# Optimization experiments

Hardware: AMD Instinct MI355X
Metric: run time of the kernel (lower is better)

## Reference

```python
import jax, jax.numpy as jnp
import numpy as np

SHIFTS = (1, 2)          # _GLOBAL_SHIFTS, all < channels so none filtered
LN_EPS = 1e-5


def _layernorm(x, g, b):
    mu = jnp.mean(x, axis=-1, keepdims=True)
    var = jnp.var(x, axis=-1, keepdims=True)
    return (x - mu) * jax.lax.rsqrt(var + LN_EPS) * g + b


def setup_inputs() -> dict:
    key = jax.random.key(0)
    ks = jax.random.split(key, 4)
    B, H, W, D = 8, 96, 96, 256
    n_comp = 2 * len(SHIFTS)  # full mode: dot + wedge per shift
    x = jax.random.normal(ks[0], (B, H, W, D), dtype=jnp.float32)
    # glorot-uniform style scaling for the two dense kernels
    pk = jax.random.normal(ks[1], (n_comp * D, D), dtype=jnp.float32) * (1.0 / np.sqrt(n_comp * D))
    gk = jax.random.normal(ks[2], (2 * D, D), dtype=jnp.float32) * (1.0 / np.sqrt(2 * D))
    return {
        "x": x,
        "ln_gamma": jnp.ones((D,), jnp.float32),
        "ln_beta": jnp.zeros((D,), jnp.float32),
        "proj_kernel": pk,
        "proj_bias": jnp.zeros((D,), jnp.float32),
        "gate_kernel": gk,
        "gate_bias": jnp.zeros((D,), jnp.float32),
        "gamma": jnp.full((D,), 1e-5, jnp.float32),  # LayerScale init
    }


def reference(x, ln_gamma, ln_beta, proj_kernel, proj_bias,
              gate_kernel, gate_bias, gamma):
    # ---- pre-norm ----
    h_norm = _layernorm(x, ln_gamma, ln_beta)                 # [B,H,W,D]
    # ---- context stream (ctx_mode='diff'): deviation from spatial mean ----
    z_det = h_norm
    z_ctx = h_norm - jnp.mean(h_norm, axis=(1, 2), keepdims=True)
    # ---- sparse rolling Clifford product (cli_mode='full') ----
    feats = []
    for s in SHIFTS:
        ctx_s = jnp.roll(z_ctx, -s, axis=-1)   # Z_ctx[(c+s) % D]
        det_s = jnp.roll(z_det, -s, axis=-1)   # Z_det[(c+s) % D]
        dot = jax.nn.silu(z_det * ctx_s)                      # inner part
        wedge = z_det * ctx_s - z_ctx * det_s                 # bivector part
        feats.append(dot)
        feats.append(wedge)
    feats = jnp.concatenate(feats, axis=-1)                   # [B,H,W,4D]
    g_feat = feats @ proj_kernel + proj_bias                  # [B,H,W,D]
    # ---- gated geometric residual ----
    gate_in = jnp.concatenate([h_norm, g_feat], axis=-1)      # [B,H,W,2D]
    alpha = jax.nn.sigmoid(gate_in @ gate_kernel + gate_bias)
    h_mix = (jax.nn.silu(h_norm) + alpha * g_feat) * gamma    # LayerScale
    # drop_path_rate == 0.0 -> identity; caller-side residual add
    return x + h_mix
```

## Files before the change

### kernel.cpp

```cpp
#include <hip/hip_runtime.h>
#include <hip/hip_bf16.h>

typedef unsigned short u16;
typedef unsigned int   u32;
typedef __attribute__((ext_vector_type(2))) u32   u32x2;
typedef __attribute__((ext_vector_type(4))) float f32x4;
typedef __attribute__((ext_vector_type(4))) u32   u32x4;
typedef __attribute__((ext_vector_type(8))) short bf16x8;

#define HWPIX  9216
#define NPIX   73728
#define LN_EPS 1e-5f
#define MROW   64
#define HSTR   264
#define ASTR   40

template<int N> struct IC { static constexpr int value = N; };

__device__ __forceinline__ u16 f2bf(float f){
  u32 u = __builtin_bit_cast(u32, f);
  u += 0x7fffu + ((u >> 16) & 1u);
  return (u16)(u >> 16);
}
__device__ __forceinline__ u32 pkbf(float lo, float hi){
  u32 d;
  asm("v_cvt_pk_bf16_f32 %0, %1, %2" : "=v"(d) : "v"(lo), "v"(hi));
  return d;
}
__device__ __forceinline__ float lo2f(u32 w){ return __builtin_bit_cast(float, w << 16); }
__device__ __forceinline__ float hi2f(u32 w){ return __builtin_bit_cast(float, w & 0xffff0000u); }
__device__ __forceinline__ float bfu2f(u16 h){ return __builtin_bit_cast(float, (u32)h << 16); }
__device__ __forceinline__ float fsigmoid(float v){ return __fdividef(1.f, 1.f + __expf(-v)); }
__device__ __forceinline__ float fsilu(float v){ return __fdividef(v, 1.f + __expf(-v)); }

__device__ __forceinline__ void gld16(const u16* g, u16* l){
  __builtin_amdgcn_global_load_lds((const __attribute__((address_space(1))) void*)g,
                                   (__attribute__((address_space(3))) void*)l,
                                   16, 0, 0);
}

__global__ __launch_bounds__(256) void wconv(const float* __restrict__ pk,
                                             const float* __restrict__ gk,
                                             u16* __restrict__ wsdot,
                                             u16* __restrict__ wsgate)
{
  int gid = blockIdx.x * 256 + threadIdx.x;
  int t = gid >> 10, S = gid & 1023;
  int q = (S >> 2) & 15, pp = S & 3, w8 = (S >> 6) & 7, rb = S >> 9;
  int n  = rb * 128 + w8 * 16 + q;
  int kq = pp ^ ((q >> 1) & 3);
  const float* W; int k0; u16* dst;
  if (t < 8)       { W = pk; k0 =       t      * 32 + kq * 8; dst = wsdot  + (size_t)t * 8192; }
  else if (t < 16) { W = pk; k0 = 512 + (t-8)  * 32 + kq * 8; dst = wsdot  + (size_t)t * 8192; }
  else             { W = gk; k0 =       (t-16) * 32 + kq * 8; dst = wsgate + (size_t)(t-16) * 8192; }
  u32 ow[4];
  #pragma unroll
  for (int e = 0; e < 4; ++e) {
    float f0 = W[(size_t)(k0 + 2*e)     * 256 + n];
    float f1 = W[(size_t)(k0 + 2*e + 1) * 256 + n];
    ow[e] = (u32)f2bf(f0) | ((u32)f2bf(f1) << 16);
  }
  *(u32x4*)(dst + (size_t)S * 8) = (u32x4){ow[0], ow[1], ow[2], ow[3]};
}

__global__ __launch_bounds__(256) void ln_partial(const float* __restrict__ x,
                                                  const float* __restrict__ g,
                                                  const float* __restrict__ bt,
                                                  float* __restrict__ partial)
{
  const int bh = blockIdx.x;
  const int tid = threadIdx.x;
  const int wv = tid >> 6, lane = tid & 63;
  const float* xrow = x + (size_t)bh * 96 * 256;
  __shared__ float red[4][256];

  f32x4 gv = *(const f32x4*)(g  + lane * 4);
  f32x4 bv = *(const f32x4*)(bt + lane * 4);
  f32x4 acc = {0.f, 0.f, 0.f, 0.f};

  for (int w = wv; w < 96; w += 4) {
    f32x4 v = *(const f32x4*)(xrow + w * 256 + lane * 4);
    float s  = v[0] + v[1] + v[2] + v[3];
    float s2 = v[0]*v[0] + v[1]*v[1] + v[2]*v[2] + v[3]*v[3];
    #pragma unroll
    for (int m = 1; m < 64; m <<= 1) { s += __shfl_xor(s, m); s2 += __shfl_xor(s2, m); }
    float mu  = s * (1.f / 256.f);
    float var = s2 * (1.f / 256.f) - mu * mu;
    float rs  = rsqrtf(var + LN_EPS);
    #pragma unroll
    for (int j = 0; j < 4; ++j) acc[j] += (v[j] - mu) * rs * gv[j] + bv[j];
  }
  *(f32x4*)(&red[wv][lane * 4]) = acc;
  __syncthreads();
  float s = red[0][tid] + red[1][tid] + red[2][tid] + red[3][tid];
  partial[(size_t)bh * 256 + tid] = s;
}

__global__ __launch_bounds__(256) void ln_mean(const float* __restrict__ partial,
                                               float* __restrict__ mean)
{
  int b = blockIdx.x, c = threadIdx.x;
  float s = 0.f;
  for (int h = 0; h < 96; ++h) s += partial[((size_t)b * 96 + h) * 256 + c];
  float m = s * (1.f / 9216.f);
  mean[b * 258 + c] = m;
  if (c < 2) mean[b * 258 + 256 + c] = m;
}

__global__ __launch_bounds__(256) void wfold(const float* __restrict__ pk,
                                             const float* __restrict__ meang,
                                             u16* __restrict__ wsW)
{
  __shared__ float msh[256];
  int gid = blockIdx.x * 256 + threadIdx.x;
  int chunk = gid >> 10;
  int b = chunk >> 3, j = chunk & 7;
  msh[threadIdx.x] = meang[b * 258 + threadIdx.x];
  __syncthreads();
  int S = gid & 1023;
  int q = (S >> 2) & 15, pp = S & 3, w8 = (S >> 6) & 7, rb = S >> 9;
  int n  = rb * 128 + w8 * 16 + q;
  int kq = pp ^ ((q >> 1) & 3);
  u32 ow[4];
  #pragma unroll
  for (int e = 0; e < 4; ++e) {
    float r[2];
    #pragma unroll
    for (int hh = 0; hh < 2; ++hh) {
      int c = j * 32 + kq * 8 + 2 * e + hh;
      int cm1 = (c + 255) & 255, cm2 = (c + 254) & 255;
      int cp1 = (c + 1) & 255,   cp2 = (c + 2) & 255;
      r[hh] = msh[cm1] * pk[(size_t)(256 + cm1) * 256 + n]
            - msh[cp1] * pk[(size_t)(256 + c)   * 256 + n]
            + msh[cm2] * pk[(size_t)(768 + cm2) * 256 + n]
            - msh[cp2] * pk[(size_t)(768 + c)   * 256 + n];
    }
    ow[e] = (u32)f2bf(r[0]) | ((u32)f2bf(r[1]) << 16);
  }
  *(u32x4*)(wsW + (size_t)chunk * 8192 + (size_t)S * 8) = (u32x4){ow[0], ow[1], ow[2], ow[3]};
}

__global__ __launch_bounds__(512, 4) void fused(
    const float* __restrict__ x,
    const float* __restrict__ lng, const float* __restrict__ lnb,
    const u16* __restrict__ wsdot, const u16* __restrict__ wsW,
    const u16* __restrict__ wsgate,
    const float* __restrict__ pbias, const float* __restrict__ gbias,
    const float* __restrict__ gamma, const float* __restrict__ meang,
    float* __restrict__ out)
{
  __shared__ u16 hn[MROW * HSTR];
  __shared__ u16 afg[2][MROW * ASTR];
  __shared__ u16 Bl [2][8192];
  __shared__ float msh[258];

  const int tid  = threadIdx.x;
  const long pix0 = (long)blockIdx.x * MROW;
  const int bat  = (int)(pix0 / HWPIX);

  const int wave = tid >> 6, lane = tid & 63;
  const int wr = wave & 1, wc = wave >> 1;
  const int fr = lane & 15, kq = lane >> 4;
  const int bswz = (kq ^ ((fr >> 1) & 3)) * 8;
  const int br = tid >> 3, bo = (tid & 7) * 4;

  f32x4 acc[2][4];
  #pragma unroll
  for (int i = 0; i < 2; ++i)
    #pragma unroll
    for (int j = 0; j < 4; ++j) acc[i][j] = (f32x4){0.f, 0.f, 0.f, 0.f};
  u32 gfp[2][4][2];

  auto sgptr = [&](auto SG) -> const u16* {
    constexpr int sg = decltype(SG)::value;
    if constexpr      (sg == 0) return wsdot;
    else if constexpr (sg == 1) return wsdot + 8 * 8192;
    else if constexpr (sg == 2) return wsW + (size_t)bat * 65536;
    else if constexpr (sg == 3) return wsgate;
    else                        return wsgate + 8 * 8192;
  };
  auto stageB = [&](auto UC, int buf) {
    constexpr int u = decltype(UC)::value;
    const u16* src = sgptr(IC<(u >> 3)>{}) + (size_t)(u & 7) * 8192 + tid * 8;
    u16* dst = &Bl[buf][wave * 512];
    gld16(src, dst);
    gld16(src + 4096, dst + 4096);
  };

  stageB(IC<0>{}, 0);

  if (tid < 258) msh[tid] = meang[bat * 258 + tid];

  float pbv[4];
  #pragma unroll
  for (int nt = 0; nt < 4; ++nt) pbv[nt] = pbias[wc * 64 + nt * 16 + fr];

  {
    const int p = tid >> 3, o = tid & 7;
    const float* xp = x + (pix0 + p) * 256 + o * 32;
    float s = 0.f, s2 = 0.f;
    #pragma unroll
    for (int i = 0; i < 8; ++i) {
      f32x4 v = *(const f32x4*)(xp + i * 4);
      s  += v[0] + v[1] + v[2] + v[3];
      s2 += v[0]*v[0] + v[1]*v[1] + v[2]*v[2] + v[3]*v[3];
    }
    s += __shfl_xor(s, 1); s2 += __shfl_xor(s2, 1);
    s += __shfl_xor(s, 2); s2 += __shfl_xor(s2, 2);
    s += __shfl_xor(s, 4); s2 += __shfl_xor(s2, 4);
    float mu  = s * (1.f / 256.f);
    float var = s2 * (1.f / 256.f) - mu * mu;
    float rs  = rsqrtf(var + LN_EPS);

    const float* gp = lng + o * 32;
    const float* bp = lnb + o * 32;
    u16* zd = hn + p * HSTR + o * 32;
    #pragma unroll
    for (int i = 0; i < 8; ++i) {
      f32x4 v  = *(const f32x4*)(xp + i * 4);
      f32x4 gg = *(const f32x4*)(gp + i * 4);
      f32x4 bb = *(const f32x4*)(bp + i * 4);
      float h0 = (v[0] - mu) * rs * gg[0] + bb[0];
      float h1 = (v[1] - mu) * rs * gg[1] + bb[1];
      float h2 = (v[2] - mu) * rs * gg[2] + bb[2];
      float h3 = (v[3] - mu) * rs * gg[3] + bb[3];
      u32 d0 = pkbf(h0, h1);
      u32 d1 = pkbf(h2, h3);
      *(u32*)(zd + i * 4)     = d0;
      *(u32*)(zd + i * 4 + 2) = d1;
      if (i == 0 && o == 0) *(u32*)(hn + p * HSTR + 256) = d0;
    }
  }

  auto featsD = [&](auto SC, int w, int buf) {
    constexpr int s = decltype(SC)::value;
    const int cc = w * 32 + bo;
    const u16* zp = hn + br * HSTR + cc;
    u32x2 aa = *(const u32x2*)(zp);
    u32 a2   = *(const u32*)(zp + 4);
    float h0 = lo2f(aa[0]), h1 = hi2f(aa[0]), h2 = lo2f(aa[1]);
    float h3 = hi2f(aa[1]), h4 = lo2f(a2), h5 = hi2f(a2);
    float m0 = msh[cc + s], m1 = msh[cc + s + 1];
    float m2 = msh[cc + s + 2], m3 = msh[cc + s + 3];
    float t0, t1, t2, t3;
    if constexpr (s == 1) { t0 = h1; t1 = h2; t2 = h3; t3 = h4; }
    else                  { t0 = h2; t1 = h3; t2 = h4; t3 = h5; }
    float r0 = fsilu(h0 * (t0 - m0));
    float r1 = fsilu(h1 * (t1 - m1));
    float r2 = fsilu(h2 * (t2 - m2));
    float r3 = fsilu(h3 * (t3 - m3));
    *(u32*)(&afg[buf][br * ASTR + bo])     = pkbf(r0, r1);
    *(u32*)(&afg[buf][br * ASTR + bo + 2]) = pkbf(r2, r3);
  };

  auto gfcopy = [&](auto CGC, int buf) {
    constexpr int cg = decltype(CGC)::value;
    constexpr int par = cg & 1;
    if (wc == (cg >> 1)) {
      #pragma unroll
      for (int v = 0; v < 2; ++v) {
        #pragma unroll
        for (int ai = 0; ai < 2; ++ai)
          #pragma unroll
          for (int rp = 0; rp < 2; ++rp) {
            u32 pw = gfp[ai][par * 2 + v][rp];
            int row0 = wr * 32 + ai * 16 + kq * 4 + rp * 2;
            afg[buf][row0 * ASTR + v * 16 + fr]       = (u16)pw;
            afg[buf][(row0 + 1) * ASTR + v * 16 + fr] = (u16)(pw >> 16);
          }
      }
    }
  };

  auto domfma = [&](const u16* abase, int astr, int buf) {
    bf16x8 av0 = *(const bf16x8*)(abase);
    bf16x8 av1 = *(const bf16x8*)(abase + 16 * astr);
    const u16* bp = &Bl[buf][wc * 2048 + fr * 32 + bswz];
    __builtin_amdgcn_s_setprio(1);
    #pragma unroll
    for (int nt = 0; nt < 4; ++nt) {
      bf16x8 bv = *(const bf16x8*)(bp + nt * 512);
      acc[0][nt] = __builtin_amdgcn_mfma_f32_16x16x32_bf16(av0, bv, acc[0][nt], 0, 0, 0);
      acc[1][nt] = __builtin_amdgcn_mfma_f32_16x16x32_bf16(av1, bv, acc[1][nt], 0, 0, 0);
    }
    __builtin_amdgcn_s_setprio(0);
  };

  asm volatile("s_waitcnt vmcnt(0) lgkmcnt(0)" ::: "memory");
  __builtin_amdgcn_s_barrier();
  featsD(IC<1>{}, 0, 0);
  asm volatile("s_waitcnt lgkmcnt(0)" ::: "memory");
  __builtin_amdgcn_s_barrier();

  auto stepfn = [&](auto SEGC, auto JC) {
    constexpr int SEG = decltype(SEGC)::value;
    constexpr int j   = decltype(JC)::value;
    constexpr int t   = SEG * 8 + j;
    constexpr int cb  = t & 1, nb = cb ^ 1;
    constexpr int u   = t + 1;
    if constexpr (u < 40) stageB(IC<u>{}, nb);
    if constexpr (SEG == 0 || SEG == 1 || SEG == 4)
      domfma(&afg[cb][(wr * 32 + fr) * ASTR + kq * 8], ASTR, cb);
    else
      domfma(&hn[(wr * 32 + fr) * HSTR + j * 32 + kq * 8], HSTR, cb);
    constexpr int useg = u >> 3;
    if constexpr (u < 40) {
      if constexpr      (useg == 0) featsD(IC<1>{}, u & 7, nb);
      else if constexpr (useg == 1) featsD(IC<2>{}, u & 7, nb);
      else if constexpr (useg == 4) gfcopy(IC<u - 32>{}, nb);
    }
    if constexpr (t == 23) {
      #pragma unroll
      for (int nt = 0; nt < 4; ++nt)
        #pragma unroll
        for (int ai = 0; ai < 2; ++ai) {
          f32x4 a = acc[ai][nt];
          gfp[ai][nt][0] = pkbf(a[0] + pbv[nt], a[1] + pbv[nt]);
          gfp[ai][nt][1] = pkbf(a[2] + pbv[nt], a[3] + pbv[nt]);
          acc[ai][nt] = (f32x4){0.f, 0.f, 0.f, 0.f};
        }
    }
    asm volatile("s_waitcnt vmcnt(0) lgkmcnt(0)" ::: "memory");
    __builtin_amdgcn_s_barrier();
  };
  auto runseg = [&](auto SEGC) {
    stepfn(SEGC, IC<0>{}); stepfn(SEGC, IC<1>{});
    stepfn(SEGC, IC<2>{}); stepfn(SEGC, IC<3>{});
    stepfn(SEGC, IC<4>{}); stepfn(SEGC, IC<5>{});
    stepfn(SEGC, IC<6>{}); stepfn(SEGC, IC<7>{});
  };
  runseg(IC<0>{}); runseg(IC<1>{}); runseg(IC<2>{});
  runseg(IC<3>{}); runseg(IC<4>{});

  float gbv[4], gmv[4];
  #pragma unroll
  for (int nt = 0; nt < 4; ++nt) {
    int col = wc * 64 + nt * 16 + fr;
    gbv[nt] = gbias[col]; gmv[nt] = gamma[col];
  }
  #pragma unroll
  for (int ai = 0; ai < 2; ++ai)
    #pragma unroll
    for (int rr = 0; rr < 4; ++rr) {
      const int row = wr * 32 + ai * 16 + kq * 4 + rr;
      const long pix = pix0 + row;
      #pragma unroll
      for (int nt = 0; nt < 4; ++nt) {
        int col = wc * 64 + nt * 16 + fr;
        float xv = x[pix * 256 + col];
        float hh = bfu2f(hn[row * HSTR + col]);
        u32 pw = gfp[ai][nt][rr >> 1];
        float gfv = bfu2f((u16)((rr & 1) ? (pw >> 16) : pw));
        float al = fsigmoid(acc[ai][nt][rr] + gbv[nt]);
        out[pix * 256 + col] = xv + (fsilu(hh) + al * gfv) * gmv[nt];
      }
    }
}

extern "C" void kernel_launch(void* const* d_in, const int* in_sizes, int n_in,
                              void* d_out, int out_size, void* d_ws, size_t ws_size,
                              hipStream_t stream) {
  const float* x     = (const float*)d_in[0];
  const float* lng   = (const float*)d_in[1];
  const float* lnb   = (const float*)d_in[2];
  const float* pk    = (const float*)d_in[3];
  const float* pbias = (const float*)d_in[4];
  const float* gk    = (const float*)d_in[5];
  const float* gbias = (const float*)d_in[6];
  const float* gamma = (const float*)d_in[7];
  float* out = (float*)d_out;

  char* ws = (char*)d_ws;
  u16*   wsdot   = (u16*)ws;
  u16*   wsgate  = (u16*)(ws + 262144);
  float* meang   = (float*)(ws + 524288);
  u16*   wsW     = (u16*)(ws + 532544);
  float* partial = (float*)(ws + 532544);

  wconv<<<128, 256, 0, stream>>>(pk, gk, wsdot, wsgate);
  ln_partial<<<768, 256, 0, stream>>>(x, lng, lnb, partial);
  ln_mean<<<8, 256, 0, stream>>>(partial, meang);
  wfold<<<256, 256, 0, stream>>>(pk, meang, wsW);
  fused<<<NPIX / MROW, 512, 0, stream>>>(x, lng, lnb, wsdot, wsW, wsgate,
                                         pbias, gbias, gamma, meang, out);
}
```

Before: 154.9 us.

## Load B fragments directly to registers and compute dot features per wave

Weight fragments are pre-permuted into MFMA lane order so each wave loads its B operands straight from global memory into registers, double-buffered, in place of staging through shared memory with global_load_lds. The silu dot features are computed in registers per wave from the normalized tile, using a pre-shifted mean table, so the shared feature buffer is used only for the gate segment. This removes most per-step block barriers and the LDS traffic for B and for the dot features. In exchange it raises register pressure and repeats global weight loads for each wave, relying on cache.

```diff
diff --git a/kernel.cpp b/kernel.cpp
--- a/kernel.cpp
+++ b/kernel.cpp
@@ -3,7 +3,6 @@
 
 typedef unsigned short u16;
 typedef unsigned int   u32;
-typedef __attribute__((ext_vector_type(2))) u32   u32x2;
 typedef __attribute__((ext_vector_type(4))) float f32x4;
 typedef __attribute__((ext_vector_type(4))) u32   u32x4;
 typedef __attribute__((ext_vector_type(8))) short bf16x8;
@@ -33,12 +32,6 @@
 __device__ __forceinline__ float fsigmoid(float v){ return __fdividef(1.f, 1.f + __expf(-v)); }
 __device__ __forceinline__ float fsilu(float v){ return __fdividef(v, 1.f + __expf(-v)); }
 
-__device__ __forceinline__ void gld16(const u16* g, u16* l){
-  __builtin_amdgcn_global_load_lds((const __attribute__((address_space(1))) void*)g,
-                                   (__attribute__((address_space(3))) void*)l,
-                                   16, 0, 0);
-}
-
 __global__ __launch_bounds__(256) void wconv(const float* __restrict__ pk,
                                              const float* __restrict__ gk,
                                              u16* __restrict__ wsdot,
@@ -46,18 +39,20 @@
 {
   int gid = blockIdx.x * 256 + threadIdx.x;
   int t = gid >> 10, S = gid & 1023;
-  int q = (S >> 2) & 15, pp = S & 3, w8 = (S >> 6) & 7, rb = S >> 9;
-  int n  = rb * 128 + w8 * 16 + q;
-  int kq = pp ^ ((q >> 1) & 3);
+  int wc = S >> 8, nt = (S >> 6) & 3, lane = S & 63;
+  int fr = lane & 15, kq = lane >> 4;
+  int n  = wc * 64 + nt * 16 + fr;
   const float* W; int k0; u16* dst;
-  if (t < 8)       { W = pk; k0 =       t      * 32 + kq * 8; dst = wsdot  + (size_t)t * 8192; }
-  else if (t < 16) { W = pk; k0 = 512 + (t-8)  * 32 + kq * 8; dst = wsdot  + (size_t)t * 8192; }
-  else             { W = gk; k0 =       (t-16) * 32 + kq * 8; dst = wsgate + (size_t)(t-16) * 8192; }
+  if (t < 8)       { W = pk; k0 =       t      * 32; dst = wsdot  + (size_t)t * 8192; }
+  else if (t < 16) { W = pk; k0 = 512 + (t-8)  * 32; dst = wsdot  + (size_t)t * 8192; }
+  else if (t < 24) { W = gk; k0 =       (t-16) * 32; dst = wsgate + (size_t)(t-16) * 8192; }
+  else             { W = gk; k0 = 256 + (t-24) * 32; dst = wsgate + (size_t)(t-24) * 8192; }
+  int kb = k0 + kq * 8;
   u32 ow[4];
   #pragma unroll
   for (int e = 0; e < 4; ++e) {
-    float f0 = W[(size_t)(k0 + 2*e)     * 256 + n];
-    float f1 = W[(size_t)(k0 + 2*e + 1) * 256 + n];
+    float f0 = W[(size_t)(kb + 2*e)     * 256 + n];
+    float f1 = W[(size_t)(kb + 2*e + 1) * 256 + n];
     ow[e] = (u32)f2bf(f0) | ((u32)f2bf(f1) << 16);
   }
   *(u32x4*)(dst + (size_t)S * 8) = (u32x4){ow[0], ow[1], ow[2], ow[3]};
@@ -118,9 +113,9 @@
   msh[threadIdx.x] = meang[b * 258 + threadIdx.x];
   __syncthreads();
   int S = gid & 1023;
-  int q = (S >> 2) & 15, pp = S & 3, w8 = (S >> 6) & 7, rb = S >> 9;
-  int n  = rb * 128 + w8 * 16 + q;
-  int kq = pp ^ ((q >> 1) & 3);
+  int wc = S >> 8, nt = (S >> 6) & 3, lane = S & 63;
+  int fr = lane & 15, kq = lane >> 4;
+  int n  = wc * 64 + nt * 16 + fr;
   u32 ow[4];
   #pragma unroll
   for (int e = 0; e < 4; ++e) {
@@ -151,8 +146,7 @@
 {
   __shared__ u16 hn[MROW * HSTR];
   __shared__ u16 afg[2][MROW * ASTR];
-  __shared__ u16 Bl [2][8192];
-  __shared__ float msh[258];
+  __shared__ float mshp[2][256];
 
   const int tid  = threadIdx.x;
   const long pix0 = (long)blockIdx.x * MROW;
@@ -161,8 +155,11 @@
   const int wave = tid >> 6, lane = tid & 63;
   const int wr = wave & 1, wc = wave >> 1;
   const int fr = lane & 15, kq = lane >> 4;
-  const int bswz = (kq ^ ((fr >> 1) & 3)) * 8;
-  const int br = tid >> 3, bo = (tid & 7) * 4;
+
+  if (tid < 256) {
+    mshp[0][tid] = meang[bat * 258 + tid + 1];
+    mshp[1][tid] = meang[bat * 258 + tid + 2];
+  }
 
   f32x4 acc[2][4];
   #pragma unroll
@@ -171,25 +168,28 @@
     for (int j = 0; j < 4; ++j) acc[i][j] = (f32x4){0.f, 0.f, 0.f, 0.f};
   u32 gfp[2][4][2];
 
-  auto sgptr = [&](auto SG) -> const u16* {
-    constexpr int sg = decltype(SG)::value;
+  u32x4 b0[4], b1[4];
+  auto sgbase = [&](auto SEGC) -> const u16* {
+    constexpr int sg = decltype(SEGC)::value;
     if constexpr      (sg == 0) return wsdot;
     else if constexpr (sg == 1) return wsdot + 8 * 8192;
     else if constexpr (sg == 2) return wsW + (size_t)bat * 65536;
     else if constexpr (sg == 3) return wsgate;
     else                        return wsgate + 8 * 8192;
   };
-  auto stageB = [&](auto UC, int buf) {
-    constexpr int u = decltype(UC)::value;
-    const u16* src = sgptr(IC<(u >> 3)>{}) + (size_t)(u & 7) * 8192 + tid * 8;
-    u16* dst = &Bl[buf][wave * 512];
-    gld16(src, dst);
-    gld16(src + 4096, dst + 4096);
-  };
-
-  stageB(IC<0>{}, 0);
-
-  if (tid < 258) msh[tid] = meang[bat * 258 + tid];
+  auto loadB = [&](auto CH) {
+    constexpr int ch = decltype(CH)::value;
+    const u16* s0 = sgbase(IC<(ch >> 3)>{}) + (size_t)(ch & 7) * 8192 + wc * 2048 + lane * 8;
+    if constexpr ((ch & 1) == 0) {
+      b0[0] = *(const u32x4*)(s0);        b0[1] = *(const u32x4*)(s0 + 512);
+      b0[2] = *(const u32x4*)(s0 + 1024); b0[3] = *(const u32x4*)(s0 + 1536);
+    } else {
+      b1[0] = *(const u32x4*)(s0);        b1[1] = *(const u32x4*)(s0 + 512);
+      b1[2] = *(const u32x4*)(s0 + 1024); b1[3] = *(const u32x4*)(s0 + 1536);
+    }
+  };
+
+  loadB(IC<0>{});
 
   float pbv[4];
   #pragma unroll
@@ -232,25 +232,33 @@
     }
   }
 
-  auto featsD = [&](auto SC, int w, int buf) {
+  auto featsRow = [&](auto SC, int w, int row) -> bf16x8 {
     constexpr int s = decltype(SC)::value;
-    const int cc = w * 32 + bo;
-    const u16* zp = hn + br * HSTR + cc;
-    u32x2 aa = *(const u32x2*)(zp);
-    u32 a2   = *(const u32*)(zp + 4);
-    float h0 = lo2f(aa[0]), h1 = hi2f(aa[0]), h2 = lo2f(aa[1]);
-    float h3 = hi2f(aa[1]), h4 = lo2f(a2), h5 = hi2f(a2);
-    float m0 = msh[cc + s], m1 = msh[cc + s + 1];
-    float m2 = msh[cc + s + 2], m3 = msh[cc + s + 3];
-    float t0, t1, t2, t3;
-    if constexpr (s == 1) { t0 = h1; t1 = h2; t2 = h3; t3 = h4; }
-    else                  { t0 = h2; t1 = h3; t2 = h4; t3 = h5; }
-    float r0 = fsilu(h0 * (t0 - m0));
-    float r1 = fsilu(h1 * (t1 - m1));
-    float r2 = fsilu(h2 * (t2 - m2));
-    float r3 = fsilu(h3 * (t3 - m3));
-    *(u32*)(&afg[buf][br * ASTR + bo])     = pkbf(r0, r1);
-    *(u32*)(&afg[buf][br * ASTR + bo + 2]) = pkbf(r2, r3);
+    const int cc = w * 32 + kq * 8;
+    const u16* zp = hn + row * HSTR + cc;
+    u32x4 hv = *(const u32x4*)(zp);
+    u32  hx  = *(const u32*)(zp + 8);
+    float h0 = lo2f(hv[0]), h1 = hi2f(hv[0]), h2 = lo2f(hv[1]), h3 = hi2f(hv[1]);
+    float h4 = lo2f(hv[2]), h5 = hi2f(hv[2]), h6 = lo2f(hv[3]), h7 = hi2f(hv[3]);
+    float h8 = lo2f(hx),  h9 = hi2f(hx);
+    const float* mp = &mshp[s - 1][cc];
+    f32x4 ma = *(const f32x4*)(mp);
+    f32x4 mb = *(const f32x4*)(mp + 4);
+    float t0, t1, t2, t3, t4, t5, t6, t7;
+    if constexpr (s == 1) { t0=h1; t1=h2; t2=h3; t3=h4; t4=h5; t5=h6; t6=h7; t7=h8; }
+    else                  { t0=h2; t1=h3; t2=h4; t3=h5; t4=h6; t5=h7; t6=h8; t7=h9; }
+    float r0 = fsilu(h0 * (t0 - ma[0]));
+    float r1 = fsilu(h1 * (t1 - ma[1]));
+    float r2 = fsilu(h2 * (t2 - ma[2]));
+    float r3 = fsilu(h3 * (t3 - ma[3]));
+    float r4 = fsilu(h4 * (t4 - mb[0]));
+    float r5 = fsilu(h5 * (t5 - mb[1]));
+    float r6 = fsilu(h6 * (t6 - mb[2]));
+    float r7 = fsilu(h7 * (t7 - mb[3]));
+    u32x4 o_;
+    o_[0] = pkbf(r0, r1); o_[1] = pkbf(r2, r3);
+    o_[2] = pkbf(r4, r5); o_[3] = pkbf(r6, r7);
+    return __builtin_bit_cast(bf16x8, o_);
   };
 
   auto gfcopy = [&](auto CGC, int buf) {
@@ -272,43 +280,43 @@
     }
   };
 
-  auto domfma = [&](const u16* abase, int astr, int buf) {
-    bf16x8 av0 = *(const bf16x8*)(abase);
-    bf16x8 av1 = *(const bf16x8*)(abase + 16 * astr);
-    const u16* bp = &Bl[buf][wc * 2048 + fr * 32 + bswz];
+  auto domfma = [&](bf16x8 av0, bf16x8 av1, auto PAR) {
     __builtin_amdgcn_s_setprio(1);
     #pragma unroll
     for (int nt = 0; nt < 4; ++nt) {
-      bf16x8 bv = *(const bf16x8*)(bp + nt * 512);
+      bf16x8 bv;
+      if constexpr (decltype(PAR)::value == 0) bv = __builtin_bit_cast(bf16x8, b0[nt]);
+      else                                     bv = __builtin_bit_cast(bf16x8, b1[nt]);
       acc[0][nt] = __builtin_amdgcn_mfma_f32_16x16x32_bf16(av0, bv, acc[0][nt], 0, 0, 0);
       acc[1][nt] = __builtin_amdgcn_mfma_f32_16x16x32_bf16(av1, bv, acc[1][nt], 0, 0, 0);
     }
     __builtin_amdgcn_s_setprio(0);
   };
 
-  asm volatile("s_waitcnt vmcnt(0) lgkmcnt(0)" ::: "memory");
-  __builtin_amdgcn_s_barrier();
-  featsD(IC<1>{}, 0, 0);
-  asm volatile("s_waitcnt lgkmcnt(0)" ::: "memory");
-  __builtin_amdgcn_s_barrier();
-
-  auto stepfn = [&](auto SEGC, auto JC) {
-    constexpr int SEG = decltype(SEGC)::value;
-    constexpr int j   = decltype(JC)::value;
-    constexpr int t   = SEG * 8 + j;
-    constexpr int cb  = t & 1, nb = cb ^ 1;
+  __syncthreads();
+
+  auto stepfn = [&](auto TC) {
+    constexpr int t   = decltype(TC)::value;
+    constexpr int seg = t >> 3, loc = t & 7;
     constexpr int u   = t + 1;
-    if constexpr (u < 40) stageB(IC<u>{}, nb);
-    if constexpr (SEG == 0 || SEG == 1 || SEG == 4)
-      domfma(&afg[cb][(wr * 32 + fr) * ASTR + kq * 8], ASTR, cb);
-    else
-      domfma(&hn[(wr * 32 + fr) * HSTR + j * 32 + kq * 8], HSTR, cb);
-    constexpr int useg = u >> 3;
-    if constexpr (u < 40) {
-      if constexpr      (useg == 0) featsD(IC<1>{}, u & 7, nb);
-      else if constexpr (useg == 1) featsD(IC<2>{}, u & 7, nb);
-      else if constexpr (useg == 4) gfcopy(IC<u - 32>{}, nb);
-    }
+    if constexpr (u < 40) loadB(IC<u>{});
+    bf16x8 av0, av1;
+    if constexpr (seg == 0) {
+      av0 = featsRow(IC<1>{}, loc, wr * 32 + fr);
+      av1 = featsRow(IC<1>{}, loc, wr * 32 + 16 + fr);
+    } else if constexpr (seg == 1) {
+      av0 = featsRow(IC<2>{}, loc, wr * 32 + fr);
+      av1 = featsRow(IC<2>{}, loc, wr * 32 + 16 + fr);
+    } else if constexpr (seg == 2 || seg == 3) {
+      const u16* ar = hn + (wr * 32 + fr) * HSTR + loc * 32 + kq * 8;
+      av0 = *(const bf16x8*)(ar);
+      av1 = *(const bf16x8*)(ar + 16 * HSTR);
+    } else {
+      const u16* ar = &afg[t & 1][(wr * 32 + fr) * ASTR + kq * 8];
+      av0 = *(const bf16x8*)(ar);
+      av1 = *(const bf16x8*)(ar + 16 * ASTR);
+    }
+    domfma(av0, av1, IC<t & 1>{});
     if constexpr (t == 23) {
       #pragma unroll
       for (int nt = 0; nt < 4; ++nt)
@@ -320,17 +328,17 @@
           acc[ai][nt] = (f32x4){0.f, 0.f, 0.f, 0.f};
         }
     }
-    asm volatile("s_waitcnt vmcnt(0) lgkmcnt(0)" ::: "memory");
-    __builtin_amdgcn_s_barrier();
-  };
-  auto runseg = [&](auto SEGC) {
-    stepfn(SEGC, IC<0>{}); stepfn(SEGC, IC<1>{});
-    stepfn(SEGC, IC<2>{}); stepfn(SEGC, IC<3>{});
-    stepfn(SEGC, IC<4>{}); stepfn(SEGC, IC<5>{});
-    stepfn(SEGC, IC<6>{}); stepfn(SEGC, IC<7>{});
-  };
-  runseg(IC<0>{}); runseg(IC<1>{}); runseg(IC<2>{});
-  runseg(IC<3>{}); runseg(IC<4>{});
+    if constexpr (t >= 31 && t < 39) {
+      gfcopy(IC<t - 31>{}, (t + 1) & 1);
+      __syncthreads();
+    }
+  };
+  auto run8 = [&](auto B8) {
+    constexpr int b8 = decltype(B8)::value;
+    stepfn(IC<b8 + 0>{}); stepfn(IC<b8 + 1>{}); stepfn(IC<b8 + 2>{}); stepfn(IC<b8 + 3>{});
+    stepfn(IC<b8 + 4>{}); stepfn(IC<b8 + 5>{}); stepfn(IC<b8 + 6>{}); stepfn(IC<b8 + 7>{});
+  };
+  run8(IC<0>{}); run8(IC<8>{}); run8(IC<16>{}); run8(IC<24>{}); run8(IC<32>{});
 
   float gbv[4], gmv[4];
   #pragma unroll
```

Measured after the change: 270.6 us. 74.7% more time.

## Recompute LN on the fly from precomputed stats and triple-buffer weight staging

Applied to the files above, without the earlier changes.

The prep kernel now also writes each pixel's LayerNorm mean and rsqrt to the workspace. The fused kernel no longer keeps a bf16 copy of the normalized tile in LDS; it reloads x from global memory for each 32-column slice and renormalizes it with the stored stats. The freed LDS goes to a three-slot weight buffer that prefetches two stages ahead, waiting with vmcnt(2) instead of draining all loads at each barrier. The occupancy hint drops from 4 to 2, and x is read repeatedly from global or cache in exchange for less LDS and deeper overlap of weight loads.

```diff
diff --git a/kernel.cpp b/kernel.cpp
--- a/kernel.cpp
+++ b/kernel.cpp
@@ -3,7 +3,7 @@
 
 typedef unsigned short u16;
 typedef unsigned int   u32;
-typedef __attribute__((ext_vector_type(2))) u32   u32x2;
+typedef __attribute__((ext_vector_type(2))) float f32x2;
 typedef __attribute__((ext_vector_type(4))) float f32x4;
 typedef __attribute__((ext_vector_type(4))) u32   u32x4;
 typedef __attribute__((ext_vector_type(8))) short bf16x8;
@@ -12,7 +12,6 @@
 #define NPIX   73728
 #define LN_EPS 1e-5f
 #define MROW   64
-#define HSTR   264
 #define ASTR   40
 
 template<int N> struct IC { static constexpr int value = N; };
@@ -27,8 +26,6 @@
   asm("v_cvt_pk_bf16_f32 %0, %1, %2" : "=v"(d) : "v"(lo), "v"(hi));
   return d;
 }
-__device__ __forceinline__ float lo2f(u32 w){ return __builtin_bit_cast(float, w << 16); }
-__device__ __forceinline__ float hi2f(u32 w){ return __builtin_bit_cast(float, w & 0xffff0000u); }
 __device__ __forceinline__ float bfu2f(u16 h){ return __builtin_bit_cast(float, (u32)h << 16); }
 __device__ __forceinline__ float fsigmoid(float v){ return __fdividef(1.f, 1.f + __expf(-v)); }
 __device__ __forceinline__ float fsilu(float v){ return __fdividef(v, 1.f + __expf(-v)); }
@@ -63,10 +60,11 @@
   *(u32x4*)(dst + (size_t)S * 8) = (u32x4){ow[0], ow[1], ow[2], ow[3]};
 }
 
-__global__ __launch_bounds__(256) void ln_partial(const float* __restrict__ x,
-                                                  const float* __restrict__ g,
-                                                  const float* __restrict__ bt,
-                                                  float* __restrict__ partial)
+__global__ __launch_bounds__(256) void prep(const float* __restrict__ x,
+                                            const float* __restrict__ g,
+                                            const float* __restrict__ bt,
+                                            float* __restrict__ mu_rs,
+                                            float* __restrict__ partial)
 {
   const int bh = blockIdx.x;
   const int tid = threadIdx.x;
@@ -87,6 +85,7 @@
     float mu  = s * (1.f / 256.f);
     float var = s2 * (1.f / 256.f) - mu * mu;
     float rs  = rsqrtf(var + LN_EPS);
+    if (lane == 0) *(f32x2*)(mu_rs + (size_t)(bh * 96 + w) * 2) = f32x2{mu, rs};
     #pragma unroll
     for (int j = 0; j < 4; ++j) acc[j] += (v[j] - mu) * rs * gv[j] + bv[j];
   }
@@ -140,19 +139,20 @@
   *(u32x4*)(wsW + (size_t)chunk * 8192 + (size_t)S * 8) = (u32x4){ow[0], ow[1], ow[2], ow[3]};
 }
 
-__global__ __launch_bounds__(512, 4) void fused(
+__global__ __launch_bounds__(512, 2) void fused(
     const float* __restrict__ x,
     const float* __restrict__ lng, const float* __restrict__ lnb,
     const u16* __restrict__ wsdot, const u16* __restrict__ wsW,
-    const u16* __restrict__ wsgate,
+    const u16* __restrict__ wsgate, const float* __restrict__ mu_rs,
     const float* __restrict__ pbias, const float* __restrict__ gbias,
     const float* __restrict__ gamma, const float* __restrict__ meang,
     float* __restrict__ out)
 {
-  __shared__ u16 hn[MROW * HSTR];
   __shared__ u16 afg[2][MROW * ASTR];
-  __shared__ u16 Bl [2][8192];
+  __shared__ u16 Bl [3][8192];
+  __shared__ float gshb[2][260];
   __shared__ float msh[258];
+  __shared__ float mursh[128];
 
   const int tid  = threadIdx.x;
   const long pix0 = (long)blockIdx.x * MROW;
@@ -162,97 +162,76 @@
   const int wr = wave & 1, wc = wave >> 1;
   const int fr = lane & 15, kq = lane >> 4;
   const int bswz = (kq ^ ((fr >> 1) & 3)) * 8;
-  const int br = tid >> 3, bo = (tid & 7) * 4;
-
-  f32x4 acc[2][4];
-  #pragma unroll
-  for (int i = 0; i < 2; ++i)
-    #pragma unroll
-    for (int j = 0; j < 4; ++j) acc[i][j] = (f32x4){0.f, 0.f, 0.f, 0.f};
-  u32 gfp[2][4][2];
-
-  auto sgptr = [&](auto SG) -> const u16* {
-    constexpr int sg = decltype(SG)::value;
+  const int brow = tid >> 3, o4 = (tid & 7) * 4;
+
+  auto sgbase = [&](auto SEGC) -> const u16* {
+    constexpr int sg = decltype(SEGC)::value;
     if constexpr      (sg == 0) return wsdot;
     else if constexpr (sg == 1) return wsdot + 8 * 8192;
     else if constexpr (sg == 2) return wsW + (size_t)bat * 65536;
     else if constexpr (sg == 3) return wsgate;
     else                        return wsgate + 8 * 8192;
   };
-  auto stageB = [&](auto UC, int buf) {
-    constexpr int u = decltype(UC)::value;
-    const u16* src = sgptr(IC<(u >> 3)>{}) + (size_t)(u & 7) * 8192 + tid * 8;
-    u16* dst = &Bl[buf][wave * 512];
+  auto stage = [&](auto UC, auto SL) {
+    constexpr int u  = decltype(UC)::value;
+    constexpr int sl = decltype(SL)::value;
+    const u16* src = sgbase(IC<(u >> 3)>{}) + (size_t)(u & 7) * 8192 + tid * 8;
+    u16* dst = &Bl[sl][wave * 512];
     gld16(src, dst);
     gld16(src + 4096, dst + 4096);
   };
 
-  stageB(IC<0>{}, 0);
-
+  stage(IC<0>{}, IC<0>{});
+  stage(IC<1>{}, IC<1>{});
+
+  if (tid < 256)      { gshb[0][tid] = lng[tid]; gshb[1][tid] = lnb[tid]; }
+  else if (tid < 260) { int c = tid - 256; gshb[0][256 + c] = lng[c]; gshb[1][256 + c] = lnb[c]; }
   if (tid < 258) msh[tid] = meang[bat * 258 + tid];
-
+  if (tid < 128) mursh[tid] = mu_rs[pix0 * 2 + tid];
+
+  f32x4 acc[2][4];
+  #pragma unroll
+  for (int i = 0; i < 2; ++i)
+    #pragma unroll
+    for (int j = 0; j < 4; ++j) acc[i][j] = (f32x4){0.f, 0.f, 0.f, 0.f};
+  u32 gfp[2][4][2];
   float pbv[4];
   #pragma unroll
   for (int nt = 0; nt < 4; ++nt) pbv[nt] = pbias[wc * 64 + nt * 16 + fr];
 
-  {
-    const int p = tid >> 3, o = tid & 7;
-    const float* xp = x + (pix0 + p) * 256 + o * 32;
-    float s = 0.f, s2 = 0.f;
-    #pragma unroll
-    for (int i = 0; i < 8; ++i) {
-      f32x4 v = *(const f32x4*)(xp + i * 4);
-      s  += v[0] + v[1] + v[2] + v[3];
-      s2 += v[0]*v[0] + v[1]*v[1] + v[2]*v[2] + v[3]*v[3];
-    }
-    s += __shfl_xor(s, 1); s2 += __shfl_xor(s2, 1);
-    s += __shfl_xor(s, 2); s2 += __shfl_xor(s2, 2);
-    s += __shfl_xor(s, 4); s2 += __shfl_xor(s2, 4);
-    float mu  = s * (1.f / 256.f);
-    float var = s2 * (1.f / 256.f) - mu * mu;
-    float rs  = rsqrtf(var + LN_EPS);
-
-    const float* gp = lng + o * 32;
-    const float* bp = lnb + o * 32;
-    u16* zd = hn + p * HSTR + o * 32;
-    #pragma unroll
-    for (int i = 0; i < 8; ++i) {
-      f32x4 v  = *(const f32x4*)(xp + i * 4);
-      f32x4 gg = *(const f32x4*)(gp + i * 4);
-      f32x4 bb = *(const f32x4*)(bp + i * 4);
-      float h0 = (v[0] - mu) * rs * gg[0] + bb[0];
-      float h1 = (v[1] - mu) * rs * gg[1] + bb[1];
-      float h2 = (v[2] - mu) * rs * gg[2] + bb[2];
-      float h3 = (v[3] - mu) * rs * gg[3] + bb[3];
-      u32 d0 = pkbf(h0, h1);
-      u32 d1 = pkbf(h2, h3);
-      *(u32*)(zd + i * 4)     = d0;
-      *(u32*)(zd + i * 4 + 2) = d1;
-      if (i == 0 && o == 0) *(u32*)(hn + p * HSTR + 256) = d0;
-    }
-  }
-
-  auto featsD = [&](auto SC, int w, int buf) {
+  __syncthreads();
+
+  const float* xrowp = x + (pix0 + brow) * 256;
+  const float muv = mursh[brow * 2];
+  const float rsv = mursh[brow * 2 + 1];
+
+  auto featsB = [&](auto SC, int w, int buf) {
     constexpr int s = decltype(SC)::value;
-    const int cc = w * 32 + bo;
-    const u16* zp = hn + br * HSTR + cc;
-    u32x2 aa = *(const u32x2*)(zp);
-    u32 a2   = *(const u32*)(zp + 4);
-    float h0 = lo2f(aa[0]), h1 = hi2f(aa[0]), h2 = lo2f(aa[1]);
-    float h3 = hi2f(aa[1]), h4 = lo2f(a2), h5 = hi2f(a2);
-    float m0 = msh[cc + s], m1 = msh[cc + s + 1];
-    float m2 = msh[cc + s + 2], m3 = msh[cc + s + 3];
-    float t0, t1, t2, t3;
-    if constexpr (s == 1) { t0 = h1; t1 = h2; t2 = h3; t3 = h4; }
-    else                  { t0 = h2; t1 = h3; t2 = h4; t3 = h5; }
-    float r0 = fsilu(h0 * (t0 - m0));
-    float r1 = fsilu(h1 * (t1 - m1));
-    float r2 = fsilu(h2 * (t2 - m2));
-    float r3 = fsilu(h3 * (t3 - m3));
-    *(u32*)(&afg[buf][br * ASTR + bo])     = pkbf(r0, r1);
-    *(u32*)(&afg[buf][br * ASTR + bo + 2]) = pkbf(r2, r3);
-  };
-
+    const int cc = w * 32 + o4;
+    f32x4 xa = *(const f32x4*)(xrowp + cc);
+    f32x4 xb = (cc == 252) ? *(const f32x4*)(xrowp) : *(const f32x4*)(xrowp + cc + 4);
+    float h[8];
+    #pragma unroll
+    for (int j = 0; j < 4; ++j) h[j]     = (xa[j] - muv) * rsv * gshb[0][cc + j]     + gshb[1][cc + j];
+    #pragma unroll
+    for (int j = 0; j < 4; ++j) h[4 + j] = (xb[j] - muv) * rsv * gshb[0][cc + 4 + j] + gshb[1][cc + 4 + j];
+    float r0 = fsilu(h[0] * (h[0 + s] - msh[cc + s]));
+    float r1 = fsilu(h[1] * (h[1 + s] - msh[cc + 1 + s]));
+    float r2 = fsilu(h[2] * (h[2 + s] - msh[cc + 2 + s]));
+    float r3 = fsilu(h[3] * (h[3 + s] - msh[cc + 3 + s]));
+    *(u32*)(&afg[buf][brow * ASTR + o4])     = pkbf(r0, r1);
+    *(u32*)(&afg[buf][brow * ASTR + o4 + 2]) = pkbf(r2, r3);
+  };
+  auto hB = [&](int w, int buf) {
+    const int cc = w * 32 + o4;
+    f32x4 xa = *(const f32x4*)(xrowp + cc);
+    float h0 = (xa[0] - muv) * rsv * gshb[0][cc]     + gshb[1][cc];
+    float h1 = (xa[1] - muv) * rsv * gshb[0][cc + 1] + gshb[1][cc + 1];
+    float h2 = (xa[2] - muv) * rsv * gshb[0][cc + 2] + gshb[1][cc + 2];
+    float h3 = (xa[3] - muv) * rsv * gshb[0][cc + 3] + gshb[1][cc + 3];
+    *(u32*)(&afg[buf][brow * ASTR + o4])     = pkbf(h0, h1);
+    *(u32*)(&afg[buf][brow * ASTR + o4 + 2]) = pkbf(h2, h3);
+  };
   auto gfcopy = [&](auto CGC, int buf) {
     constexpr int cg = decltype(CGC)::value;
     constexpr int par = cg & 1;
@@ -272,10 +251,12 @@
     }
   };
 
-  auto domfma = [&](const u16* abase, int astr, int buf) {
-    bf16x8 av0 = *(const bf16x8*)(abase);
-    bf16x8 av1 = *(const bf16x8*)(abase + 16 * astr);
-    const u16* bp = &Bl[buf][wc * 2048 + fr * 32 + bswz];
+  auto domfma = [&](auto AB, auto SL) {
+    constexpr int ab = decltype(AB)::value, sl = decltype(SL)::value;
+    const u16* ar = &afg[ab][(wr * 32 + fr) * ASTR + kq * 8];
+    bf16x8 av0 = *(const bf16x8*)(ar);
+    bf16x8 av1 = *(const bf16x8*)(ar + 16 * ASTR);
+    const u16* bp = &Bl[sl][wc * 2048 + fr * 32 + bswz];
     __builtin_amdgcn_s_setprio(1);
     #pragma unroll
     for (int nt = 0; nt < 4; ++nt) {
@@ -286,29 +267,18 @@
     __builtin_amdgcn_s_setprio(0);
   };
 
-  asm volatile("s_waitcnt vmcnt(0) lgkmcnt(0)" ::: "memory");
-  __builtin_amdgcn_s_barrier();
-  featsD(IC<1>{}, 0, 0);
+  featsB(IC<1>{}, 0, 0);
   asm volatile("s_waitcnt lgkmcnt(0)" ::: "memory");
   __builtin_amdgcn_s_barrier();
 
-  auto stepfn = [&](auto SEGC, auto JC) {
-    constexpr int SEG = decltype(SEGC)::value;
-    constexpr int j   = decltype(JC)::value;
-    constexpr int t   = SEG * 8 + j;
-    constexpr int cb  = t & 1, nb = cb ^ 1;
-    constexpr int u   = t + 1;
-    if constexpr (u < 40) stageB(IC<u>{}, nb);
-    if constexpr (SEG == 0 || SEG == 1 || SEG == 4)
-      domfma(&afg[cb][(wr * 32 + fr) * ASTR + kq * 8], ASTR, cb);
-    else
-      domfma(&hn[(wr * 32 + fr) * HSTR + j * 32 + kq * 8], HSTR, cb);
-    constexpr int useg = u >> 3;
-    if constexpr (u < 40) {
-      if constexpr      (useg == 0) featsD(IC<1>{}, u & 7, nb);
-      else if constexpr (useg == 1) featsD(IC<2>{}, u & 7, nb);
-      else if constexpr (useg == 4) gfcopy(IC<u - 32>{}, nb);
-    }
+  auto stepfn = [&](auto TC) {
+    constexpr int t = decltype(TC)::value;
+    constexpr int u = t + 1;
+    if constexpr (u < 8)       featsB(IC<1>{}, u & 7, u & 1);
+    else if constexpr (u < 16) featsB(IC<2>{}, u & 7, u & 1);
+    else if constexpr (u < 32) hB(u & 7, u & 1);
+    else if constexpr (u < 40) gfcopy(IC<u - 32>{}, u & 1);
+    domfma(IC<t & 1>{}, IC<t % 3>{});
     if constexpr (t == 23) {
       #pragma unroll
       for (int nt = 0; nt < 4; ++nt)
@@ -320,17 +290,17 @@
           acc[ai][nt] = (f32x4){0.f, 0.f, 0.f, 0.f};
         }
     }
-    asm volatile("s_waitcnt vmcnt(0) lgkmcnt(0)" ::: "memory");
+    if constexpr (t + 2 < 40) stage(IC<t + 2>{}, IC<(t + 2) % 3>{});
+    if constexpr (t < 37) asm volatile("s_waitcnt vmcnt(2) lgkmcnt(0)" ::: "memory");
+    else                  asm volatile("s_waitcnt vmcnt(0) lgkmcnt(0)" ::: "memory");
     __builtin_amdgcn_s_barrier();
   };
-  auto runseg = [&](auto SEGC) {
-    stepfn(SEGC, IC<0>{}); stepfn(SEGC, IC<1>{});
-    stepfn(SEGC, IC<2>{}); stepfn(SEGC, IC<3>{});
-    stepfn(SEGC, IC<4>{}); stepfn(SEGC, IC<5>{});
-    stepfn(SEGC, IC<6>{}); stepfn(SEGC, IC<7>{});
-  };
-  runseg(IC<0>{}); runseg(IC<1>{}); runseg(IC<2>{});
-  runseg(IC<3>{}); runseg(IC<4>{});
+  auto run8 = [&](auto B8) {
+    constexpr int b8 = decltype(B8)::value;
+    stepfn(IC<b8 + 0>{}); stepfn(IC<b8 + 1>{}); stepfn(IC<b8 + 2>{}); stepfn(IC<b8 + 3>{});
+    stepfn(IC<b8 + 4>{}); stepfn(IC<b8 + 5>{}); stepfn(IC<b8 + 6>{}); stepfn(IC<b8 + 7>{});
+  };
+  run8(IC<0>{}); run8(IC<8>{}); run8(IC<16>{}); run8(IC<24>{}); run8(IC<32>{});
 
   float gbv[4], gmv[4];
   #pragma unroll
@@ -344,11 +314,12 @@
     for (int rr = 0; rr < 4; ++rr) {
       const int row = wr * 32 + ai * 16 + kq * 4 + rr;
       const long pix = pix0 + row;
+      const float mu2 = mursh[row * 2], rs2 = mursh[row * 2 + 1];
       #pragma unroll
       for (int nt = 0; nt < 4; ++nt) {
         int col = wc * 64 + nt * 16 + fr;
         float xv = x[pix * 256 + col];
-        float hh = bfu2f(hn[row * HSTR + col]);
+        float hh = (xv - mu2) * rs2 * gshb[0][col] + gshb[1][col];
         u32 pw = gfp[ai][nt][rr >> 1];
         float gfv = bfu2f((u16)((rr & 1) ? (pw >> 16) : pw));
         float al = fsigmoid(acc[ai][nt][rr] + gbv[nt]);
@@ -376,11 +347,12 @@
   float* meang   = (float*)(ws + 524288);
   u16*   wsW     = (u16*)(ws + 532544);
   float* partial = (float*)(ws + 532544);
+  float* mu_rs   = (float*)(ws + 1581120);
 
   wconv<<<128, 256, 0, stream>>>(pk, gk, wsdot, wsgate);
-  ln_partial<<<768, 256, 0, stream>>>(x, lng, lnb, partial);
+  prep<<<768, 256, 0, stream>>>(x, lng, lnb, mu_rs, partial);
   ln_mean<<<8, 256, 0, stream>>>(partial, meang);
   wfold<<<256, 256, 0, stream>>>(pk, meang, wsW);
-  fused<<<NPIX / MROW, 512, 0, stream>>>(x, lng, lnb, wsdot, wsW, wsgate,
+  fused<<<NPIX / MROW, 512, 0, stream>>>(x, lng, lnb, wsdot, wsW, wsgate, mu_rs,
                                          pbias, gbias, gamma, meang, out);
 }
```

Result: faster. 151.3 us (-2.4%).
